# Performance work log

Hardware: AMD Instinct MI355X
Metric: run time of the kernel (lower is better)

Reference implementation:

```python
import jax, jax.numpy as jnp
import numpy as np
import math

B, C, IMG_H, IMG_W = 64, 3, 224, 224
P = 14                 # patches per side
PH = PW = 16           # patch size
D = 768                # hidden_d (= C*PH*PW = input_d)
L = 12                 # n_blocks
NH = 12                # n_heads
DH = D // NH           # d_head = 64
FF = 4 * D             # mlp hidden
S = P * P + 1          # 197 tokens (cls + patches)
EXTRACT = (2, 5, 8, 11)
LN_EPS = 1e-5


def _sinusoidal_pos(seq_len, d):
    pos = np.arange(seq_len, dtype=np.float32)[:, None]
    div = np.exp(np.arange(0, d, 2, dtype=np.float32) * -(math.log(10000.0) / d))
    out = np.zeros((seq_len, d), dtype=np.float32)
    out[:, 0::2] = np.sin(pos * div)
    out[:, 1::2] = np.cos(pos * div)
    return jnp.asarray(out)


def setup_inputs() -> dict:
    key = jax.random.key(0)
    ks = jax.random.split(key, 12)
    sc = 0.02
    return {
        "images": jax.random.normal(ks[0], (B, C, IMG_H, IMG_W), jnp.float32),
        "mapper_w": jax.random.normal(ks[1], (D, D), jnp.float32) * sc,  # input_d == D
        "mapper_b": jnp.zeros((D,), jnp.float32),
        "cls_token": jax.random.uniform(ks[2], (1, D), jnp.float32),
        "pos_emb": _sinusoidal_pos(S, D),
        "ln1_g": jnp.ones((L, D), jnp.float32),
        "ln1_b": jnp.zeros((L, D), jnp.float32),
        "qw": jax.random.normal(ks[3], (L, NH, DH, DH), jnp.float32) * sc,
        "qb": jnp.zeros((L, NH, DH), jnp.float32),
        "kw": jax.random.normal(ks[4], (L, NH, DH, DH), jnp.float32) * sc,
        "kb": jnp.zeros((L, NH, DH), jnp.float32),
        "vw": jax.random.normal(ks[5], (L, NH, DH, DH), jnp.float32) * sc,
        "vb": jnp.zeros((L, NH, DH), jnp.float32),
        "ow": jax.random.normal(ks[6], (L, D, D), jnp.float32) * sc,
        "ob": jnp.zeros((L, D), jnp.float32),
        "ln2_g": jnp.ones((L, D), jnp.float32),
        "ln2_b": jnp.zeros((L, D), jnp.float32),
        "mlp_w1": jax.random.normal(ks[7], (L, FF, D), jnp.float32) * sc,
        "mlp_b1": jnp.zeros((L, FF), jnp.float32),
        "mlp_w2": jax.random.normal(ks[8], (L, D, FF), jnp.float32) * sc,
        "mlp_b2": jnp.zeros((L, D), jnp.float32),
    }


def _layernorm(x, g, b):
    mu = jnp.mean(x, axis=-1, keepdims=True)
    var = jnp.mean(jnp.square(x - mu), axis=-1, keepdims=True)
    return (x - mu) * jax.lax.rsqrt(var + LN_EPS) * g + b


def reference(images, mapper_w, mapper_b, cls_token, pos_emb,
              ln1_g, ln1_b, qw, qb, kw, kb, vw, vb, ow, ob,
              ln2_g, ln2_b, mlp_w1, mlp_b1, mlp_w2, mlp_b2):
    n = images.shape[0]
    # patchify: [n,C,H,W] -> [n, P*P, C*PH*PW]
    patches = images.reshape(n, C, P, PH, P, PW)
    patches = patches.transpose(0, 2, 4, 1, 3, 5).reshape(n, P * P, C * PH * PW)
    tokens = patches @ mapper_w.T + mapper_b                      # [n, P*P, D]
    cls = jnp.broadcast_to(cls_token[None], (n, 1, D))
    x = jnp.concatenate([cls, tokens], axis=1) + pos_emb[None]    # [n, S, D]

    extracted = []
    for i in range(L):
        # --- MHSA (note: scale is d_head**2, as in the source) ---
        h = _layernorm(x, ln1_g[i], ln1_b[i])
        hh = h.reshape(n, S, NH, DH)
        q = jnp.einsum('bshd,hed->bshe', hh, qw[i]) + qb[i]
        k = jnp.einsum('bshd,hed->bshe', hh, kw[i]) + kb[i]
        v = jnp.einsum('bshd,hed->bshe', hh, vw[i]) + vb[i]
        scores = jnp.einsum('bqhe,bkhe->bhqk', q, k) / (DH ** 2)
        attn = jax.nn.softmax(scores, axis=-1)
        ctx = jnp.einsum('bhqk,bkhe->bqhe', attn, v).reshape(n, S, D)
        x = x + ctx @ ow[i].T + ob[i]
        # --- MLP ---
        h2 = _layernorm(x, ln2_g[i], ln2_b[i])
        mid = jax.nn.gelu(h2 @ mlp_w1[i].T + mlp_b1[i], approximate=False)
        x = x + mid @ mlp_w2[i].T + mlp_b2[i]
        if i in EXTRACT:
            extracted.append(x)
    return jnp.stack(extracted)  # [4, n, S, D]
```

## Files before the change

### kernel.cpp

```cpp
#include <hip/hip_runtime.h>
#include <hip/hip_bf16.h>
#include <math.h>

static constexpr int NB   = 64;
static constexpr int SS   = 197;
static constexpr int DD   = 768;
static constexpr int NHH  = 12;
static constexpr int DHH  = 64;
static constexpr int FFF  = 3072;
static constexpr int TOK  = NB * SS;
static constexpr int NPAT = 196;
static constexpr int PADM = 12672;
static constexpr int PADM2= 12800;
static constexpr long NX  = (long)TOK * DD;
static constexpr int APAD = 256;

typedef __attribute__((ext_vector_type(8))) short bf16x8;
typedef __attribute__((ext_vector_type(4))) float f32x4;

__device__ inline void gll16(const __hip_bfloat16* g, __hip_bfloat16* l) {
    __builtin_amdgcn_global_load_lds(
        (const __attribute__((address_space(1))) void*)g,
        (__attribute__((address_space(3))) void*)l, 16, 0, 0);
}

template<int EPI, bool OUTBF>
__global__ __launch_bounds__(256, 4) void gemm128(
    const __hip_bfloat16* __restrict__ A, int lda,
    const __hip_bfloat16* __restrict__ Bt, int ldb,
    void* __restrict__ Cout, int ldc,
    const float* __restrict__ bias,
    const float* __restrict__ Rm, int ldr,
    float* __restrict__ out2,
    int M, int N, int K)
{
    __shared__ __hip_bfloat16 sh[3][2][128 * 32];

    const int nbx = gridDim.x;
    const int nwg = nbx * gridDim.y;
    int flat = blockIdx.y * nbx + blockIdx.x;
    {
        int q = nwg >> 3, r = nwg & 7;
        int xcd = flat & 7, idx = flat >> 3;
        flat = (xcd < r ? xcd * (q + 1) : r * (q + 1) + (xcd - r) * q) + idx;
    }
    const int m0 = (flat / nbx) * 128;
    const int n0 = (flat % nbx) * 128;

    const int t = threadIdx.x;
    const int wid = t >> 6, lane = t & 63;
    const int wm = wid >> 1, wn = wid & 1;
    const int l15 = lane & 15, g0 = lane >> 4;
    const int rcol = ((g0 ^ ((l15 >> 1) & 3)) * 8);

    const int srl = t >> 2, sg = t & 3;

    auto stage = [&](int buf, int k0) {
        #pragma unroll
        for (int j = 0; j < 2; ++j) {
            int row = j * 64 + srl;
            int gs = sg ^ ((row >> 1) & 3);
            gll16(A + (long)(m0 + row) * lda + k0 + gs * 8,
                  &sh[buf][0][row * 32 + sg * 8]);
        }
        #pragma unroll
        for (int j = 0; j < 2; ++j) {
            int row = j * 64 + srl;
            int gs = sg ^ ((row >> 1) & 3);
            gll16(Bt + (long)(n0 + row) * ldb + k0 + gs * 8,
                  &sh[buf][1][row * 32 + sg * 8]);
        }
    };

    f32x4 acc[4][4] = {};
    const int NT = K >> 5;

    stage(0, 0);
    stage(1, 32);
    asm volatile("s_waitcnt vmcnt(4)" ::: "memory");
    __builtin_amdgcn_sched_barrier(0);
    __builtin_amdgcn_s_barrier();
    __builtin_amdgcn_sched_barrier(0);

    int cur = 0;
    for (int kt = 0; kt < NT; ++kt) {
        const bool st2 = (kt + 2 < NT);
        const bool w1n = (kt + 1 < NT);
        int stbuf = cur + 2; if (stbuf >= 3) stbuf -= 3;

        bf16x8 af[4], bfr[4];
        #pragma unroll
        for (int mi = 0; mi < 4; ++mi)
            af[mi] = *reinterpret_cast<const bf16x8*>(
                &sh[cur][0][(wm * 64 + mi * 16 + l15) * 32 + rcol]);
        #pragma unroll
        for (int ni = 0; ni < 4; ++ni)
            bfr[ni] = *reinterpret_cast<const bf16x8*>(
                &sh[cur][1][(wn * 64 + ni * 16 + l15) * 32 + rcol]);

        if (st2) stage(stbuf, (kt + 2) << 5);

        asm volatile("s_waitcnt lgkmcnt(0)" ::: "memory");
        __builtin_amdgcn_sched_barrier(0);
        __builtin_amdgcn_s_setprio(1);
        #pragma unroll
        for (int mi = 0; mi < 4; ++mi)
            #pragma unroll
            for (int ni = 0; ni < 4; ++ni)
                acc[mi][ni] = __builtin_amdgcn_mfma_f32_16x16x32_bf16(
                    af[mi], bfr[ni], acc[mi][ni], 0, 0, 0);
        __builtin_amdgcn_s_setprio(0);
        __builtin_amdgcn_sched_barrier(0);
        if (st2)      { asm volatile("s_waitcnt vmcnt(4)" ::: "memory"); }
        else if (w1n) { asm volatile("s_waitcnt vmcnt(0)" ::: "memory"); }
        __builtin_amdgcn_sched_barrier(0);
        __builtin_amdgcn_s_barrier();
        __builtin_amdgcn_sched_barrier(0);

        cur = (cur == 2) ? 0 : cur + 1;
    }

    #pragma unroll
    for (int mi = 0; mi < 4; ++mi) {
        #pragma unroll
        for (int r = 0; r < 4; ++r) {
            int gm = m0 + wm * 64 + mi * 16 + (lane >> 4) * 4 + r;
            if (gm >= M) continue;
            #pragma unroll
            for (int ni = 0; ni < 4; ++ni) {
                int gn = n0 + wn * 64 + ni * 16 + (lane & 15);
                float v = acc[mi][ni][r];
                if (bias) v += bias[gn];
                if (EPI == 1) v += Rm[(long)gm * ldr + gn];
                if (EPI == 2) v = 0.5f * v * (1.0f + erff(v * 0.70710678118654752f));
                if (OUTBF) {
                    ((__hip_bfloat16*)Cout)[(long)gm * ldc + gn] = __float2bfloat16(v);
                } else {
                    ((float*)Cout)[(long)gm * ldc + gn] = v;
                    if (EPI == 1 && out2) out2[(long)gm * ldc + gn] = v;
                }
            }
        }
    }
}

__global__ __launch_bounds__(256) void gemm_qkv(
    const __hip_bfloat16* __restrict__ A, int lda, long sAlo,
    const __hip_bfloat16* __restrict__ Bt, int ldb, long sBhi,
    const float* __restrict__ bias, long sbhi,
    __hip_bfloat16* __restrict__ qb_, __hip_bfloat16* __restrict__ kb_,
    __hip_bfloat16* __restrict__ vtb,
    int M, int N, int K)
{
    __shared__ __hip_bfloat16 As[128 * 64];
    __shared__ __hip_bfloat16 Bs[128 * 64];

    const int zz = blockIdx.z;
    A  += zz * sAlo;
    Bt += zz * sBhi;
    bias += zz * sbhi;

    const int t = threadIdx.x;
    const int wid = t >> 6, lane = t & 63;
    const int wm = wid >> 1, wn = wid & 1;
    const int m0 = blockIdx.y * 128, n0 = blockIdx.x * 128;

    const int srow = t >> 3;
    const int scol = (t & 7) * 8;

    f32x4 acc[4][4] = {};

    for (int k0 = 0; k0 < K; k0 += 64) {
        #pragma unroll
        for (int i = 0; i < 4; ++i) {
            const __hip_bfloat16* ga = A + (long)(m0 + i * 32 + srow) * lda + k0 + scol;
            __hip_bfloat16* la = As + (i * 256 + wid * 64) * 8;
            gll16(ga, la);
            const __hip_bfloat16* gb = Bt + (long)(n0 + i * 32 + srow) * ldb + k0 + scol;
            __hip_bfloat16* lb = Bs + (i * 256 + wid * 64) * 8;
            gll16(gb, lb);
        }
        asm volatile("s_waitcnt vmcnt(0)" ::: "memory");
        __syncthreads();

        #pragma unroll
        for (int kk = 0; kk < 2; ++kk) {
            bf16x8 af[4], bfr[4];
            #pragma unroll
            for (int mi = 0; mi < 4; ++mi)
                af[mi] = *reinterpret_cast<const bf16x8*>(
                    &As[(wm * 64 + mi * 16 + (lane & 15)) * 64 + kk * 32 + (lane >> 4) * 8]);
            #pragma unroll
            for (int ni = 0; ni < 4; ++ni)
                bfr[ni] = *reinterpret_cast<const bf16x8*>(
                    &Bs[(wn * 64 + ni * 16 + (lane & 15)) * 64 + kk * 32 + (lane >> 4) * 8]);
            #pragma unroll
            for (int mi = 0; mi < 4; ++mi)
                #pragma unroll
                for (int ni = 0; ni < 4; ++ni)
                    acc[mi][ni] = __builtin_amdgcn_mfma_f32_16x16x32_bf16(
                        af[mi], bfr[ni], acc[mi][ni], 0, 0, 0);
        }
        __syncthreads();
    }

    #pragma unroll
    for (int mi = 0; mi < 4; ++mi) {
        #pragma unroll
        for (int r = 0; r < 4; ++r) {
            int gm = m0 + wm * 64 + mi * 16 + (lane >> 4) * 4 + r;
            if (gm >= M) continue;
            int bq = gm / 197, sq = gm - bq * 197;
            #pragma unroll
            for (int ni = 0; ni < 4; ++ni) {
                int gn = n0 + wn * 64 + ni * 16 + (lane & 15);
                if (gn >= N) continue;
                float v = acc[mi][ni][r] + bias[gn];
                int c = gn >> 6, e = gn & 63;
                __hip_bfloat16 bv = __float2bfloat16(v);
                if (c == 0)      qb_[(long)gm * DD + zz * 64 + e] = bv;
                else if (c == 1) kb_[(long)gm * DD + zz * 64 + e] = bv;
                else             vtb[(((long)(bq * NHH + zz)) * 128 + e) * APAD + sq] = bv;
            }
        }
    }
}

__global__ __launch_bounds__(256) void attn_flash(
    const __hip_bfloat16* __restrict__ qbuf,
    const __hip_bfloat16* __restrict__ kbuf,
    const __hip_bfloat16* __restrict__ vt,
    __hip_bfloat16* __restrict__ ctx)
{
    constexpr int KLD = 72;
    constexpr int VLD = 232;
    constexpr int PLD = 232;
    __shared__ __hip_bfloat16 Kl[208 * KLD];
    __shared__ __hip_bfloat16 Vl[64 * VLD];
    __shared__ __hip_bfloat16 Pl[4][16 * PLD];

    const int h = blockIdx.x, b = blockIdx.y;
    const int t = threadIdx.x;
    const int w = t >> 6, lane = t & 63;
    const int l15 = lane & 15, g0 = lane >> 4;

    const long row0 = (long)b * 197;
    const int  hc   = h * 64;

    for (int task = t; task < 208 * 8; task += 256) {
        int r = task >> 3, g = task & 7;
        float4 vv = *reinterpret_cast<const float4*>(kbuf + (row0 + r) * DD + hc + g * 8);
        *reinterpret_cast<float4*>(&Kl[r * KLD + g * 8]) = vv;
    }
    const __hip_bfloat16* vsrc0 = vt + (long)(b * NHH + h) * 128 * APAD;
    for (int task = t; task < 64 * 32; task += 256) {
        int e = task >> 5, g = task & 31;
        if (g < 28) {
            float4 vv = *reinterpret_cast<const float4*>(vsrc0 + (long)e * APAD + g * 8);
            *reinterpret_cast<float4*>(&Vl[e * VLD + g * 8]) = vv;
        }
    }
    __syncthreads();

    __hip_bfloat16* Pw = Pl[w];

    for (int qc = w; qc < 13; qc += 4) {
        const int q0 = qc * 16;

        const __hip_bfloat16* qsrc = qbuf + (row0 + q0 + l15) * DD + hc + g0 * 8;
        bf16x8 qf0 = *reinterpret_cast<const bf16x8*>(qsrc);
        bf16x8 qf1 = *reinterpret_cast<const bf16x8*>(qsrc + 32);

        f32x4 sacc[13];
        #pragma unroll
        for (int n = 0; n < 13; ++n) {
            bf16x8 kf0 = *reinterpret_cast<const bf16x8*>(&Kl[(n * 16 + l15) * KLD + g0 * 8]);
            bf16x8 kf1 = *reinterpret_cast<const bf16x8*>(&Kl[(n * 16 + l15) * KLD + 32 + g0 * 8]);
            f32x4 z = {0.f, 0.f, 0.f, 0.f};
            z = __builtin_amdgcn_mfma_f32_16x16x32_bf16(qf0, kf0, z, 0, 0, 0);
            sacc[n] = __builtin_amdgcn_mfma_f32_16x16x32_bf16(qf1, kf1, z, 0, 0, 0);
        }

        const int kcol = l15;
        float lrow[4];
        #pragma unroll
        for (int r = 0; r < 4; ++r) {
            float mx = -3.0e38f;
            #pragma unroll
            for (int n = 0; n < 13; ++n) {
                float s = sacc[n][r] * (1.0f / 4096.0f);
                if (n * 16 + kcol < 197) mx = fmaxf(mx, s);
            }
            #pragma unroll
            for (int off = 1; off < 16; off <<= 1) mx = fmaxf(mx, __shfl_xor(mx, off));
            float sum = 0.f;
            #pragma unroll
            for (int n = 0; n < 14; ++n) {
                float p = 0.f;
                if (n < 13 && n * 16 + kcol < 197) {
                    p = __expf(sacc[n][r] * (1.0f / 4096.0f) - mx);
                    sum += p;
                }
                Pw[(g0 * 4 + r) * PLD + n * 16 + kcol] = __float2bfloat16(p);
            }
            #pragma unroll
            for (int off = 1; off < 16; off <<= 1) sum += __shfl_xor(sum, off);
            lrow[r] = sum;
        }

        asm volatile("s_waitcnt lgkmcnt(0)" ::: "memory");

        f32x4 pv[4] = {};
        #pragma unroll
        for (int kc = 0; kc < 7; ++kc) {
            bf16x8 pf = *reinterpret_cast<const bf16x8*>(&Pw[l15 * PLD + kc * 32 + g0 * 8]);
            #pragma unroll
            for (int ni = 0; ni < 4; ++ni) {
                bf16x8 vf = *reinterpret_cast<const bf16x8*>(&Vl[(ni * 16 + l15) * VLD + kc * 32 + g0 * 8]);
                pv[ni] = __builtin_amdgcn_mfma_f32_16x16x32_bf16(pf, vf, pv[ni], 0, 0, 0);
            }
        }

        #pragma unroll
        for (int r = 0; r < 4; ++r) {
            int q = q0 + g0 * 4 + r;
            if (q >= 197) continue;
            float inv = 1.0f / lrow[r];
            #pragma unroll
            for (int ni = 0; ni < 4; ++ni)
                ctx[(row0 + q) * DD + hc + ni * 16 + l15] = __float2bfloat16(pv[ni][r] * inv);
        }
    }
}

__global__ __launch_bounds__(256) void ln_kernel(
    const float* __restrict__ X, const float* __restrict__ g,
    const float* __restrict__ b, __hip_bfloat16* __restrict__ H)
{
    const long row = blockIdx.x;
    const float* x = X + row * DD;
    const int t = threadIdx.x;
    float v[3];
    float s = 0.f, s2 = 0.f;
    #pragma unroll
    for (int i = 0; i < 3; ++i) {
        v[i] = x[t + i * 256];
        s += v[i]; s2 += v[i] * v[i];
    }
    #pragma unroll
    for (int off = 1; off < 64; off <<= 1) {
        s  += __shfl_xor(s,  off);
        s2 += __shfl_xor(s2, off);
    }
    __shared__ float red[2][4];
    const int lane = t & 63, w = t >> 6;
    if (lane == 0) { red[0][w] = s; red[1][w] = s2; }
    __syncthreads();
    float S1 = red[0][0] + red[0][1] + red[0][2] + red[0][3];
    float S2 = red[1][0] + red[1][1] + red[1][2] + red[1][3];
    float mu  = S1 * (1.0f / 768.0f);
    float var = S2 * (1.0f / 768.0f) - mu * mu;
    float rs  = rsqrtf(var + 1e-5f);
    __hip_bfloat16* h = H + row * DD;
    #pragma unroll
    for (int i = 0; i < 3; ++i) {
        int c = t + i * 256;
        h[c] = __float2bfloat16((v[i] - mu) * rs * g[c] + b[c]);
    }
}

__global__ void patchify_kernel(const float* __restrict__ img, __hip_bfloat16* __restrict__ patches)
{
    long idx = (long)blockIdx.x * 256 + threadIdx.x;
    const long total = (long)NB * NPAT * DD;
    if (idx >= total) return;
    int k  = (int)(idx % DD);
    long mp = idx / DD;
    int p  = (int)(mp % NPAT);
    long b = mp / NPAT;
    int c = k >> 8;
    int i = (k >> 4) & 15;
    int j = k & 15;
    int pr = p / 14, pc = p % 14;
    int hh = pr * 16 + i, ww = pc * 16 + j;
    patches[idx] = __float2bfloat16(img[((b * 3 + c) * 224 + hh) * 224 + ww]);
}

__global__ void assemble_kernel(const float* __restrict__ tok, const float* __restrict__ cls,
                                const float* __restrict__ pos, float* __restrict__ X)
{
    long idx = (long)blockIdx.x * 256 + threadIdx.x;
    if (idx >= NX) return;
    int d  = (int)(idx % DD);
    long bs = idx / DD;
    int s  = (int)(bs % SS);
    long b = bs / SS;
    float v = (s == 0) ? cls[d] : tok[(b * NPAT + s - 1) * DD + d];
    X[idx] = v + pos[(long)s * DD + d];
}

__global__ void f2b_kernel(const float* __restrict__ src, __hip_bfloat16* __restrict__ dst, long n4)
{
    long i = (long)blockIdx.x * 256 + threadIdx.x;
    if (i >= n4) return;
    float4 v = *reinterpret_cast<const float4*>(&src[i * 4]);
    __hip_bfloat16 o[4] = { __float2bfloat16(v.x), __float2bfloat16(v.y),
                            __float2bfloat16(v.z), __float2bfloat16(v.w) };
    *reinterpret_cast<uint2*>(&dst[i * 4]) = *reinterpret_cast<const uint2*>(o);
}

__global__ void f2b3_kernel(const float* __restrict__ s0, __hip_bfloat16* __restrict__ d0, long c0,
                            const float* __restrict__ s1, __hip_bfloat16* __restrict__ d1, long c1,
                            const float* __restrict__ s2, __hip_bfloat16* __restrict__ d2, long c2)
{
    long i = (long)blockIdx.x * 256 + threadIdx.x;
    const float* s; __hip_bfloat16* d;
    if (i < c0)                { s = s0; d = d0; }
    else if (i < c0 + c1)      { s = s1; d = d1; i -= c0; }
    else if (i < c0 + c1 + c2) { s = s2; d = d2; i -= c0 + c1; }
    else return;
    #pragma unroll
    for (int u = 0; u < 4; ++u) {
        float4 v = *reinterpret_cast<const float4*>(&s[i * 16 + u * 4]);
        __hip_bfloat16 o[4] = { __float2bfloat16(v.x), __float2bfloat16(v.y),
                                __float2bfloat16(v.z), __float2bfloat16(v.w) };
        *reinterpret_cast<uint2*>(&d[i * 16 + u * 4]) = *reinterpret_cast<const uint2*>(o);
    }
}

__global__ void qkvpack_kernel(const float* __restrict__ qw, const float* __restrict__ kw,
                               const float* __restrict__ vw, const float* __restrict__ qb,
                               const float* __restrict__ kb, const float* __restrict__ vb,
                               __hip_bfloat16* __restrict__ W, float* __restrict__ Bv)
{
    int idx = blockIdx.x * 256 + threadIdx.x;
    if (idx >= NHH * 192 * 64) return;
    int d = idx & 63;
    int rest = idx >> 6;
    int j = rest % 192;
    int h = rest / 192;
    int c = j >> 6, e = j & 63;
    const float* src = (c == 0 ? qw : c == 1 ? kw : vw) + ((long)h * 64 + e) * 64 + d;
    W[((long)h * 256 + j) * 64 + d] = __float2bfloat16(*src);
    if (d == 0) {
        const float* sb = (c == 0 ? qb : c == 1 ? kb : vb) + h * 64 + e;
        Bv[h * 192 + j] = *sb;
    }
}

extern "C" void kernel_launch(void* const* d_in, const int* in_sizes, int n_in,
                              void* d_out, int out_size, void* d_ws, size_t ws_size,
                              hipStream_t stream)
{
    const float* images   = (const float*)d_in[0];
    const float* mapper_w = (const float*)d_in[1];
    const float* mapper_b = (const float*)d_in[2];
    const float* cls      = (const float*)d_in[3];
    const float* pos      = (const float*)d_in[4];
    const float* ln1_g    = (const float*)d_in[5];
    const float* ln1_b    = (const float*)d_in[6];
    const float* qw       = (const float*)d_in[7];
    const float* qb       = (const float*)d_in[8];
    const float* kw       = (const float*)d_in[9];
    const float* kb       = (const float*)d_in[10];
    const float* vw       = (const float*)d_in[11];
    const float* vb       = (const float*)d_in[12];
    const float* ow       = (const float*)d_in[13];
    const float* ob       = (const float*)d_in[14];
    const float* ln2_g    = (const float*)d_in[15];
    const float* ln2_b    = (const float*)d_in[16];
    const float* w1       = (const float*)d_in[17];
    const float* b1       = (const float*)d_in[18];
    const float* w2       = (const float*)d_in[19];
    const float* b2       = (const float*)d_in[20];
    float* out = (float*)d_out;

    char* p0 = (char*)d_ws;
    char* pp = p0;
    auto alloc = [&](size_t bytes) { char* r = pp; pp += (bytes + 255) & ~(size_t)255; return r; };

    float*           x      = (float*)          alloc(NX * 4);
    __hip_bfloat16*  h16    = (__hip_bfloat16*) alloc((size_t)PADM2 * DD * 2);
    __hip_bfloat16*  ctx16  = (__hip_bfloat16*) alloc((size_t)PADM2 * DD * 2);
    __hip_bfloat16*  wbuf16 = (__hip_bfloat16*) alloc((size_t)(DD*DD + (size_t)FFF*DD*2) * 2);
    __hip_bfloat16*  wqkv16 = (__hip_bfloat16*) alloc((size_t)NHH * 256 * 64 * 2);
    float*           bqkv   = (float*)          alloc((size_t)NHH * 192 * 4);
    __hip_bfloat16*  qbuf   = (__hip_bfloat16*) alloc((size_t)PADM * DD * 2);
    __hip_bfloat16*  kbuf   = (__hip_bfloat16*) alloc((size_t)PADM * DD * 2);
    __hip_bfloat16*  vt     = (__hip_bfloat16*) alloc((size_t)NB * NHH * 128 * APAD * 2);
    char*            big    = alloc((size_t)PADM2 * FFF * 2);

    if ((size_t)(pp - p0) > ws_size) return;

    __hip_bfloat16* mid16     = (__hip_bfloat16*)big;
    __hip_bfloat16* patches16 = (__hip_bfloat16*)big;
    float*          tokens    = (float*)(big + (((size_t)NB * NPAT * DD * 2 + 255) & ~(size_t)255));

    __hip_bfloat16* ow16 = wbuf16;
    __hip_bfloat16* w116 = wbuf16 + (size_t)DD * DD;
    __hip_bfloat16* w216 = w116 + (size_t)FFF * DD;

    {
        long n = (long)NB * NPAT * DD;
        patchify_kernel<<<dim3((n + 255) / 256), dim3(256), 0, stream>>>(images, patches16);
        f2b_kernel<<<dim3((DD * DD / 4 + 255) / 256), dim3(256), 0, stream>>>(mapper_w, w116, DD * DD / 4);
        gemm128<0, false><<<dim3(DD / 128, (NB * NPAT) / 128), dim3(256), 0, stream>>>(
            patches16, DD, w116, DD, tokens, DD, mapper_b, nullptr, 0, nullptr,
            NB * NPAT, DD, DD);
        assemble_kernel<<<dim3((NX + 255) / 256), dim3(256), 0, stream>>>(tokens, cls, pos, x);
    }

    const int MT = (TOK + 127) / 128;
    const long C1 = (long)DD * DD / 16, C2 = (long)FFF * DD / 16;

    for (int l = 0; l < 12; ++l) {
        f2b3_kernel<<<dim3((int)((C1 + 2 * C2 + 255) / 256)), dim3(256), 0, stream>>>(
            ow + (long)l * DD * DD, ow16, C1,
            w1 + (long)l * FFF * DD, w116, C2,
            w2 + (long)l * FFF * DD, w216, C2);
        qkvpack_kernel<<<dim3((NHH * 192 * 64 + 255) / 256), dim3(256), 0, stream>>>(
            qw + (long)l * NHH * DHH * DHH, kw + (long)l * NHH * DHH * DHH,
            vw + (long)l * NHH * DHH * DHH,
            qb + (long)l * DD, kb + (long)l * DD, vb + (long)l * DD,
            wqkv16, bqkv);

        ln_kernel<<<dim3(TOK), dim3(256), 0, stream>>>(x, ln1_g + l * DD, ln1_b + l * DD, h16);

        gemm_qkv<<<dim3(2, MT, NHH), dim3(256), 0, stream>>>(
            h16, DD, 64,
            wqkv16, 64, (long)256 * 64,
            bqkv, 192,
            qbuf, kbuf, vt,
            TOK, 192, 64);

        attn_flash<<<dim3(NHH, NB), dim3(256), 0, stream>>>(qbuf, kbuf, vt, ctx16);

        gemm128<1, false><<<dim3(DD / 128, MT), dim3(256), 0, stream>>>(
            ctx16, DD, ow16, DD, x, DD, ob + l * DD, x, DD, nullptr,
            TOK, DD, DD);

        ln_kernel<<<dim3(TOK), dim3(256), 0, stream>>>(x, ln2_g + l * DD, ln2_b + l * DD, h16);

        gemm128<2, true><<<dim3(FFF / 128, MT), dim3(256), 0, stream>>>(
            h16, DD, w116, DD, mid16, FFF, b1 + l * FFF, nullptr, 0, nullptr,
            TOK, FFF, DD);

        int slot = (l == 2) ? 0 : (l == 5) ? 1 : (l == 8) ? 2 : (l == 11) ? 3 : -1;
        float* o2 = (slot >= 0) ? out + (long)slot * NX : nullptr;
        gemm128<1, false><<<dim3(DD / 128, MT), dim3(256), 0, stream>>>(
            mid16, FFF, w216, FFF, x, DD, b2 + l * DD, x, DD, o2,
            TOK, DD, FFF);
    }
}
```

Measured before the change: 5.580 ms.

## Rework GEMM to 2-wave tiles with B fragments loaded directly into registers

The main 128x128 GEMM now runs with 2 waves of 128 threads instead of 4. Each wave owns a 64x128 slice and loads its B (weight) fragments straight from global memory into registers, double-buffered across k-steps. Only A is staged in LDS through a triple buffer, which halves LDS traffic and use but raises register pressure and may cut latency hiding. Separately, the QKV kernel now writes V in row-major layout instead of a padded transpose, and the attention kernel transposes V into LDS itself.

```diff
diff --git a/kernel.cpp b/kernel.cpp
--- a/kernel.cpp
+++ b/kernel.cpp
@@ -13,7 +13,6 @@
 static constexpr int PADM = 12672;
 static constexpr int PADM2= 12800;
 static constexpr long NX  = (long)TOK * DD;
-static constexpr int APAD = 256;
 
 typedef __attribute__((ext_vector_type(8))) short bf16x8;
 typedef __attribute__((ext_vector_type(4))) float f32x4;
@@ -25,7 +24,7 @@
 }
 
 template<int EPI, bool OUTBF>
-__global__ __launch_bounds__(256, 4) void gemm128(
+__global__ __launch_bounds__(128, 2) void gemmW(
     const __hip_bfloat16* __restrict__ A, int lda,
     const __hip_bfloat16* __restrict__ Bt, int ldb,
     void* __restrict__ Cout, int ldc,
@@ -34,7 +33,7 @@
     float* __restrict__ out2,
     int M, int N, int K)
 {
-    __shared__ __hip_bfloat16 sh[3][2][128 * 32];
+    __shared__ __hip_bfloat16 shA[3][128 * 32];
 
     const int nbx = gridDim.x;
     const int nwg = nbx * gridDim.y;
@@ -49,86 +48,114 @@
 
     const int t = threadIdx.x;
     const int wid = t >> 6, lane = t & 63;
-    const int wm = wid >> 1, wn = wid & 1;
     const int l15 = lane & 15, g0 = lane >> 4;
     const int rcol = ((g0 ^ ((l15 >> 1) & 3)) * 8);
 
     const int srl = t >> 2, sg = t & 3;
 
-    auto stage = [&](int buf, int k0) {
-        #pragma unroll
-        for (int j = 0; j < 2; ++j) {
-            int row = j * 64 + srl;
+    auto stageA = [&](int buf, int k0) {
+        #pragma unroll
+        for (int j = 0; j < 4; ++j) {
+            int row = j * 32 + srl;
             int gs = sg ^ ((row >> 1) & 3);
             gll16(A + (long)(m0 + row) * lda + k0 + gs * 8,
-                  &sh[buf][0][row * 32 + sg * 8]);
-        }
-        #pragma unroll
-        for (int j = 0; j < 2; ++j) {
-            int row = j * 64 + srl;
-            int gs = sg ^ ((row >> 1) & 3);
-            gll16(Bt + (long)(n0 + row) * ldb + k0 + gs * 8,
-                  &sh[buf][1][row * 32 + sg * 8]);
+                  &shA[buf][row * 32 + sg * 8]);
         }
     };
 
-    f32x4 acc[4][4] = {};
+    const __hip_bfloat16* bbase = Bt + (long)(n0 + l15) * ldb + g0 * 8;
+    const long bstep = (long)16 * ldb;
+
+    f32x4 acc[4][8] = {};
+    bf16x8 bA[8], bB[8], af[4];
     const int NT = K >> 5;
 
-    stage(0, 0);
-    stage(1, 32);
-    asm volatile("s_waitcnt vmcnt(4)" ::: "memory");
+    stageA(0, 0);
+    stageA(1, 32);
+    #pragma unroll
+    for (int ni = 0; ni < 8; ++ni)
+        bA[ni] = *reinterpret_cast<const bf16x8*>(bbase + ni * bstep);
+    asm volatile("s_waitcnt vmcnt(12)" ::: "memory");
     __builtin_amdgcn_sched_barrier(0);
     __builtin_amdgcn_s_barrier();
     __builtin_amdgcn_sched_barrier(0);
 
     int cur = 0;
-    for (int kt = 0; kt < NT; ++kt) {
-        const bool st2 = (kt + 2 < NT);
-        const bool w1n = (kt + 1 < NT);
-        int stbuf = cur + 2; if (stbuf >= 3) stbuf -= 3;
-
-        bf16x8 af[4], bfr[4];
-        #pragma unroll
-        for (int mi = 0; mi < 4; ++mi)
-            af[mi] = *reinterpret_cast<const bf16x8*>(
-                &sh[cur][0][(wm * 64 + mi * 16 + l15) * 32 + rcol]);
-        #pragma unroll
-        for (int ni = 0; ni < 4; ++ni)
-            bfr[ni] = *reinterpret_cast<const bf16x8*>(
-                &sh[cur][1][(wn * 64 + ni * 16 + l15) * 32 + rcol]);
-
-        if (st2) stage(stbuf, (kt + 2) << 5);
-
-        asm volatile("s_waitcnt lgkmcnt(0)" ::: "memory");
-        __builtin_amdgcn_sched_barrier(0);
-        __builtin_amdgcn_s_setprio(1);
-        #pragma unroll
-        for (int mi = 0; mi < 4; ++mi)
-            #pragma unroll
-            for (int ni = 0; ni < 4; ++ni)
-                acc[mi][ni] = __builtin_amdgcn_mfma_f32_16x16x32_bf16(
-                    af[mi], bfr[ni], acc[mi][ni], 0, 0, 0);
-        __builtin_amdgcn_s_setprio(0);
-        __builtin_amdgcn_sched_barrier(0);
-        if (st2)      { asm volatile("s_waitcnt vmcnt(4)" ::: "memory"); }
-        else if (w1n) { asm volatile("s_waitcnt vmcnt(0)" ::: "memory"); }
-        __builtin_amdgcn_sched_barrier(0);
-        __builtin_amdgcn_s_barrier();
-        __builtin_amdgcn_sched_barrier(0);
-
-        cur = (cur == 2) ? 0 : cur + 1;
+    for (int kt = 0; kt < NT; kt += 2) {
+        {
+            const bool st = (kt + 2 < NT);
+            #pragma unroll
+            for (int ni = 0; ni < 8; ++ni)
+                bB[ni] = *reinterpret_cast<const bf16x8*>(bbase + ni * bstep + (kt + 1) * 32);
+            int stbuf = cur + 2; if (stbuf >= 3) stbuf -= 3;
+            if (st) stageA(stbuf, (kt + 2) << 5);
+            #pragma unroll
+            for (int mi = 0; mi < 4; ++mi)
+                af[mi] = *reinterpret_cast<const bf16x8*>(
+                    &shA[cur][(wid * 64 + mi * 16 + l15) * 32 + rcol]);
+            asm volatile("s_waitcnt lgkmcnt(0)" ::: "memory");
+            __builtin_amdgcn_sched_barrier(0);
+            __builtin_amdgcn_s_setprio(1);
+            #pragma unroll
+            for (int mi = 0; mi < 4; ++mi)
+                #pragma unroll
+                for (int ni = 0; ni < 8; ++ni)
+                    acc[mi][ni] = __builtin_amdgcn_mfma_f32_16x16x32_bf16(
+                        af[mi], bA[ni], acc[mi][ni], 0, 0, 0);
+            __builtin_amdgcn_s_setprio(0);
+            __builtin_amdgcn_sched_barrier(0);
+            if (st) { asm volatile("s_waitcnt vmcnt(12)" ::: "memory"); }
+            else    { asm volatile("s_waitcnt vmcnt(8)"  ::: "memory"); }
+            __builtin_amdgcn_sched_barrier(0);
+            __builtin_amdgcn_s_barrier();
+            __builtin_amdgcn_sched_barrier(0);
+            cur = (cur == 2) ? 0 : cur + 1;
+        }
+        {
+            const int k1 = kt + 1;
+            const bool w1 = (k1 + 1 < NT);
+            const bool st = (k1 + 2 < NT);
+            if (w1) {
+                #pragma unroll
+                for (int ni = 0; ni < 8; ++ni)
+                    bA[ni] = *reinterpret_cast<const bf16x8*>(bbase + ni * bstep + (k1 + 1) * 32);
+            }
+            int stbuf = cur + 2; if (stbuf >= 3) stbuf -= 3;
+            if (st) stageA(stbuf, (k1 + 2) << 5);
+            #pragma unroll
+            for (int mi = 0; mi < 4; ++mi)
+                af[mi] = *reinterpret_cast<const bf16x8*>(
+                    &shA[cur][(wid * 64 + mi * 16 + l15) * 32 + rcol]);
+            asm volatile("s_waitcnt lgkmcnt(0)" ::: "memory");
+            __builtin_amdgcn_sched_barrier(0);
+            __builtin_amdgcn_s_setprio(1);
+            #pragma unroll
+            for (int mi = 0; mi < 4; ++mi)
+                #pragma unroll
+                for (int ni = 0; ni < 8; ++ni)
+                    acc[mi][ni] = __builtin_amdgcn_mfma_f32_16x16x32_bf16(
+                        af[mi], bB[ni], acc[mi][ni], 0, 0, 0);
+            __builtin_amdgcn_s_setprio(0);
+            __builtin_amdgcn_sched_barrier(0);
+            if (st)      { asm volatile("s_waitcnt vmcnt(12)" ::: "memory"); }
+            else if (w1) { asm volatile("s_waitcnt vmcnt(8)"  ::: "memory"); }
+            else         { asm volatile("s_waitcnt vmcnt(0)"  ::: "memory"); }
+            __builtin_amdgcn_sched_barrier(0);
+            __builtin_amdgcn_s_barrier();
+            __builtin_amdgcn_sched_barrier(0);
+            cur = (cur == 2) ? 0 : cur + 1;
+        }
     }
 
     #pragma unroll
     for (int mi = 0; mi < 4; ++mi) {
         #pragma unroll
         for (int r = 0; r < 4; ++r) {
-            int gm = m0 + wm * 64 + mi * 16 + (lane >> 4) * 4 + r;
+            int gm = m0 + wid * 64 + mi * 16 + g0 * 4 + r;
             if (gm >= M) continue;
             #pragma unroll
-            for (int ni = 0; ni < 4; ++ni) {
-                int gn = n0 + wn * 64 + ni * 16 + (lane & 15);
+            for (int ni = 0; ni < 8; ++ni) {
+                int gn = n0 + ni * 16 + l15;
                 float v = acc[mi][ni][r];
                 if (bias) v += bias[gn];
                 if (EPI == 1) v += Rm[(long)gm * ldr + gn];
@@ -149,7 +176,7 @@
     const __hip_bfloat16* __restrict__ Bt, int ldb, long sBhi,
     const float* __restrict__ bias, long sbhi,
     __hip_bfloat16* __restrict__ qb_, __hip_bfloat16* __restrict__ kb_,
-    __hip_bfloat16* __restrict__ vtb,
+    __hip_bfloat16* __restrict__ vb_,
     int M, int N, int K)
 {
     __shared__ __hip_bfloat16 As[128 * 64];
@@ -210,7 +237,6 @@
         for (int r = 0; r < 4; ++r) {
             int gm = m0 + wm * 64 + mi * 16 + (lane >> 4) * 4 + r;
             if (gm >= M) continue;
-            int bq = gm / 197, sq = gm - bq * 197;
             #pragma unroll
             for (int ni = 0; ni < 4; ++ni) {
                 int gn = n0 + wn * 64 + ni * 16 + (lane & 15);
@@ -218,9 +244,8 @@
                 float v = acc[mi][ni][r] + bias[gn];
                 int c = gn >> 6, e = gn & 63;
                 __hip_bfloat16 bv = __float2bfloat16(v);
-                if (c == 0)      qb_[(long)gm * DD + zz * 64 + e] = bv;
-                else if (c == 1) kb_[(long)gm * DD + zz * 64 + e] = bv;
-                else             vtb[(((long)(bq * NHH + zz)) * 128 + e) * APAD + sq] = bv;
+                __hip_bfloat16* dst = (c == 0) ? qb_ : (c == 1) ? kb_ : vb_;
+                dst[(long)gm * DD + zz * 64 + e] = bv;
             }
         }
     }
@@ -229,7 +254,7 @@
 __global__ __launch_bounds__(256) void attn_flash(
     const __hip_bfloat16* __restrict__ qbuf,
     const __hip_bfloat16* __restrict__ kbuf,
-    const __hip_bfloat16* __restrict__ vt,
+    const __hip_bfloat16* __restrict__ vbuf,
     __hip_bfloat16* __restrict__ ctx)
 {
     constexpr int KLD = 72;
@@ -252,13 +277,18 @@
         float4 vv = *reinterpret_cast<const float4*>(kbuf + (row0 + r) * DD + hc + g * 8);
         *reinterpret_cast<float4*>(&Kl[r * KLD + g * 8]) = vv;
     }
-    const __hip_bfloat16* vsrc0 = vt + (long)(b * NHH + h) * 128 * APAD;
-    for (int task = t; task < 64 * 32; task += 256) {
-        int e = task >> 5, g = task & 31;
-        if (g < 28) {
-            float4 vv = *reinterpret_cast<const float4*>(vsrc0 + (long)e * APAD + g * 8);
-            *reinterpret_cast<float4*>(&Vl[e * VLD + g * 8]) = vv;
-        }
+    const __hip_bfloat16 bz = __float2bfloat16(0.0f);
+    for (int task = t; task < 64 * 27; task += 256) {
+        int e = task / 27, c = 197 + (task - e * 27);
+        Vl[e * VLD + c] = bz;
+    }
+    for (int task = t; task < 197 * 8; task += 256) {
+        int r = task >> 3, g = task & 7;
+        union { float4 f; __hip_bfloat16 hx[8]; } u;
+        u.f = *reinterpret_cast<const float4*>(vbuf + (row0 + r) * DD + hc + g * 8);
+        #pragma unroll
+        for (int j = 0; j < 8; ++j)
+            Vl[(g * 8 + j) * VLD + r] = u.hx[j];
     }
     __syncthreads();
 
@@ -487,7 +517,7 @@
     float*           bqkv   = (float*)          alloc((size_t)NHH * 192 * 4);
     __hip_bfloat16*  qbuf   = (__hip_bfloat16*) alloc((size_t)PADM * DD * 2);
     __hip_bfloat16*  kbuf   = (__hip_bfloat16*) alloc((size_t)PADM * DD * 2);
-    __hip_bfloat16*  vt     = (__hip_bfloat16*) alloc((size_t)NB * NHH * 128 * APAD * 2);
+    __hip_bfloat16*  vbuf   = (__hip_bfloat16*) alloc((size_t)PADM * DD * 2);
     char*            big    = alloc((size_t)PADM2 * FFF * 2);
 
     if ((size_t)(pp - p0) > ws_size) return;
@@ -504,7 +534,7 @@
         long n = (long)NB * NPAT * DD;
         patchify_kernel<<<dim3((n + 255) / 256), dim3(256), 0, stream>>>(images, patches16);
         f2b_kernel<<<dim3((DD * DD / 4 + 255) / 256), dim3(256), 0, stream>>>(mapper_w, w116, DD * DD / 4);
-        gemm128<0, false><<<dim3(DD / 128, (NB * NPAT) / 128), dim3(256), 0, stream>>>(
+        gemmW<0, false><<<dim3(DD / 128, (NB * NPAT) / 128), dim3(128), 0, stream>>>(
             patches16, DD, w116, DD, tokens, DD, mapper_b, nullptr, 0, nullptr,
             NB * NPAT, DD, DD);
         assemble_kernel<<<dim3((NX + 255) / 256), dim3(256), 0, stream>>>(tokens, cls, pos, x);
@@ -530,24 +560,24 @@
             h16, DD, 64,
             wqkv16, 64, (long)256 * 64,
             bqkv, 192,
-            qbuf, kbuf, vt,
+            qbuf, kbuf, vbuf,
             TOK, 192, 64);
 
-        attn_flash<<<dim3(NHH, NB), dim3(256), 0, stream>>>(qbuf, kbuf, vt, ctx16);
-
-        gemm128<1, false><<<dim3(DD / 128, MT), dim3(256), 0, stream>>>(
+        attn_flash<<<dim3(NHH, NB), dim3(256), 0, stream>>>(qbuf, kbuf, vbuf, ctx16);
+
+        gemmW<1, false><<<dim3(DD / 128, MT), dim3(128), 0, stream>>>(
             ctx16, DD, ow16, DD, x, DD, ob + l * DD, x, DD, nullptr,
             TOK, DD, DD);
 
         ln_kernel<<<dim3(TOK), dim3(256), 0, stream>>>(x, ln2_g + l * DD, ln2_b + l * DD, h16);
 
-        gemm128<2, true><<<dim3(FFF / 128, MT), dim3(256), 0, stream>>>(
+        gemmW<2, true><<<dim3(FFF / 128, MT), dim3(128), 0, stream>>>(
             h16, DD, w116, DD, mid16, FFF, b1 + l * FFF, nullptr, 0, nullptr,
             TOK, FFF, DD);
 
         int slot = (l == 2) ? 0 : (l == 5) ? 1 : (l == 8) ? 2 : (l == 11) ? 3 : -1;
         float* o2 = (slot >= 0) ? out + (long)slot * NX : nullptr;
-        gemm128<1, false><<<dim3(DD / 128, MT), dim3(256), 0, stream>>>(
+        gemmW<1, false><<<dim3(DD / 128, MT), dim3(128), 0, stream>>>(
             mid16, FFF, w216, FFF, x, DD, b2 + l * DD, x, DD, o2,
             TOK, DD, FFF);
     }
```

Result: slower. 8.294 ms (+48.6%).
